# Performance work log

Hardware: AMD Instinct MI355X
Metric: run time of the kernel (lower is better)

Reference implementation:

```python
import jax, jax.numpy as jnp
import numpy as np

B, IN, E, H, MO, OUT, K = 32768, 512, 8, 128, 256, 2, 2


def setup_inputs() -> dict:
    key = jax.random.key(0)
    ks = jax.random.split(key, 9)
    g = lambda k, shape, fan: (jax.random.normal(k, shape, jnp.float32) / np.sqrt(fan)).astype(jnp.float32)
    return {
        "num_prop": jax.random.normal(ks[0], (B, IN), jnp.float32),
        "cat_prop": jax.random.normal(ks[1], (B, 3), jnp.float32),
        "w_gate": g(ks[2], (IN, E), IN),
        "W1": g(ks[3], (E, IN, H), IN),
        "b1": jnp.zeros((E, H), jnp.float32),
        "W2": g(ks[4], (E, H, MO), H),
        "b2": jnp.zeros((E, MO), jnp.float32),
        "Wout": g(ks[5], (MO, OUT), MO),
        "bout": jnp.zeros((OUT,), jnp.float32),
    }


def _cv_squared(v):
    # torch.var is unbiased (ddof=1); eps = 1e-10
    return jnp.var(v, ddof=1) / (jnp.mean(v) ** 2 + 1e-10)


def reference(num_prop, cat_prop, w_gate, W1, b1, W2, b2, Wout, bout):
    b = num_prop.shape[0]
    x = num_prop  # eval mode: dropout is identity, gating noise disabled
    # --- top-k gating ---
    logits = x @ w_gate                                   # [B, E]
    top_vals, top_idx = jax.lax.top_k(logits, K)          # [B, K]
    gate_vals = jax.nn.softmax(top_vals, axis=-1)         # softmax over top-k logits
    gates = jnp.zeros_like(logits).at[jnp.arange(b)[:, None], top_idx].add(gate_vals)  # [B, E]
    # --- load-balancing loss ---
    importance = gates.sum(axis=0)                        # [E]
    load = (gates > 0).astype(jnp.float32).sum(axis=0)    # [E]
    loss = (_cv_squared(importance) + _cv_squared(load)) * 1e-2
    # --- experts (dense-equivalent: gates zero out non-selected experts) ---
    h = jax.nn.relu(jnp.einsum('bi,eih->beh', x, W1) + b1)          # [B, E, H]
    eo = jax.nn.softmax(jnp.einsum('beh,ehm->bem', h, W2) + b2, axis=-1)  # [B, E, MO]
    y = jnp.einsum('be,bem->bm', gates, eo)               # [B, MO]
    # --- output head ---
    out = y @ Wout + bout                                 # [B, OUT]
    return out, loss
```

## Files before the change

### kernel.cpp

```cpp
#include <hip/hip_runtime.h>

#define BN 32768
#define IN 512
#define NE 8
#define NH 128
#define MO 256

typedef const __attribute__((address_space(1))) unsigned int gu32;
typedef __attribute__((address_space(3))) unsigned int lu32;
typedef __attribute__((ext_vector_type(8))) short bf16x8;
typedef __attribute__((ext_vector_type(4))) float f32x4;

__device__ __forceinline__ void cp16(const float* g, float* l) {
    __builtin_amdgcn_global_load_lds((gu32*)g, (lu32*)l, 16, 0, 0);
}

__device__ __forceinline__ unsigned short f2bf(float f) {
    unsigned int u = __float_as_uint(f);
    u = (u + 0x7fffu + ((u >> 16) & 1u)) >> 16;
    return (unsigned short)u;
}
__device__ __forceinline__ float bf2f(unsigned short h) {
    return __uint_as_float((unsigned int)h << 16);
}

__global__ __launch_bounds__(256) void gate_kernel(
    const float* __restrict__ x, const float* __restrict__ wg,
    int* __restrict__ gcount, int* __restrict__ gload, float* __restrict__ gimp,
    int* __restrict__ idx_list, float* __restrict__ gate_list,
    float* __restrict__ out, const float* __restrict__ bout)
{
    __shared__ __align__(16) char wb[32768];
    __shared__ int counts_s[NE];
    __shared__ int load_s[NE];
    __shared__ float imp_s[NE];
    __shared__ int base_s[NE];
    __shared__ int rec_e[128];
    __shared__ int rec_p[128];
    __shared__ float rec_g[128];

    int tid = threadIdx.x;
    if (tid < NE) { counts_s[tid] = 0; load_s[tid] = 0; imp_s[tid] = 0.f; }
    if (tid < 128) {
        int row = blockIdx.x * 64 + (tid >> 1);
        out[row * 2 + (tid & 1)] = bout[tid & 1];
    }
    for (int idx = tid; idx < 1024; idx += 256) {
        int ks = idx >> 6, ls = idx & 63;
        int col = ls & 15;
        int kb = 32 * ks + 8 * (ls >> 4);
        unsigned int ph[4], pl[4];
        #pragma unroll
        for (int j = 0; j < 4; ++j) {
            float v0 = (col < 8) ? wg[(kb + 2 * j) * NE + col] : 0.f;
            float v1 = (col < 8) ? wg[(kb + 2 * j + 1) * NE + col] : 0.f;
            unsigned short h0 = f2bf(v0), h1 = f2bf(v1);
            unsigned short l0 = f2bf(v0 - bf2f(h0)), l1 = f2bf(v1 - bf2f(h1));
            ph[j] = (unsigned int)h0 | ((unsigned int)h1 << 16);
            pl[j] = (unsigned int)l0 | ((unsigned int)l1 << 16);
        }
        *(int4*)(wb + ks * 1024 + ls * 16) = make_int4(ph[0], ph[1], ph[2], ph[3]);
        *(int4*)(wb + 16384 + ks * 1024 + ls * 16) = make_int4(pl[0], pl[1], pl[2], pl[3]);
    }
    __syncthreads();

    int w = tid >> 6, l = tid & 63;
    int e = l & 15;
    int rowA = blockIdx.x * 64 + w * 16 + e;
    const float* px = x + (size_t)rowA * IN + 8 * (l >> 4);

    f32x4 acc = {};
    #pragma unroll
    for (int ks = 0; ks < 16; ++ks) {
        float4 qa = *(const float4*)(px + 32 * ks);
        float4 qb = *(const float4*)(px + 32 * ks + 4);
        float v[8] = {qa.x, qa.y, qa.z, qa.w, qb.x, qb.y, qb.z, qb.w};
        bf16x8 ah, al;
        #pragma unroll
        for (int i = 0; i < 8; ++i) {
            unsigned short h = f2bf(v[i]);
            ah[i] = (short)h;
            al[i] = (short)f2bf(v[i] - bf2f(h));
        }
        bf16x8 bh = *(const bf16x8*)(wb + ks * 1024 + l * 16);
        bf16x8 bl = *(const bf16x8*)(wb + 16384 + ks * 1024 + l * 16);
        acc = __builtin_amdgcn_mfma_f32_16x16x32_bf16(ah, bh, acc, 0, 0, 0);
        acc = __builtin_amdgcn_mfma_f32_16x16x32_bf16(ah, bl, acc, 0, 0, 0);
        acc = __builtin_amdgcn_mfma_f32_16x16x32_bf16(al, bh, acc, 0, 0, 0);
    }

    #pragma unroll
    for (int reg = 0; reg < 4; ++reg) {
        int rloc = w * 16 + 4 * (l >> 4) + reg;
        int row = blockIdx.x * 64 + rloc;
        float lv = (e < 8) ? acc[reg] : -1e30f;

        float v0 = lv; int e0 = e;
        #pragma unroll
        for (int m = 1; m < 8; m <<= 1) {
            float vo = __shfl_xor(v0, m, 64);
            int eo = __shfl_xor(e0, m, 64);
            if (vo > v0 || (vo == v0 && eo < e0)) { v0 = vo; e0 = eo; }
        }
        float v1 = (e == e0 || e >= 8) ? -1e30f : lv; int e1 = e;
        #pragma unroll
        for (int m = 1; m < 8; m <<= 1) {
            float vo = __shfl_xor(v1, m, 64);
            int eo = __shfl_xor(e1, m, 64);
            if (vo > v1 || (vo == v1 && eo < e1)) { v1 = vo; e1 = eo; }
        }
        float v2 = (e == e0 || e == e1 || e >= 8) ? -1e30f : lv;
        #pragma unroll
        for (int m = 1; m < 8; m <<= 1) v2 = fmaxf(v2, __shfl_xor(v2, m, 64));

        double dv0 = v0, dv1 = v1;
        int f0 = e0, f1 = e1;
        if (e < 8 && v1 - v2 < 2e-4f) {
            const float* xr = x + (size_t)row * IN;
            double d0 = 0, d1 = 0, d2 = 0, d3 = 0;
            for (int k = 0; k < IN; k += 4) {
                float4 xv = *(const float4*)(xr + k);
                d0 = fma((double)xv.x, (double)wg[(k    ) * NE + e], d0);
                d1 = fma((double)xv.y, (double)wg[(k + 1) * NE + e], d1);
                d2 = fma((double)xv.z, (double)wg[(k + 2) * NE + e], d2);
                d3 = fma((double)xv.w, (double)wg[(k + 3) * NE + e], d3);
            }
            double ad = (d0 + d1) + (d2 + d3);
            double w0 = ad; int g0i = e;
            #pragma unroll
            for (int m = 1; m < 8; m <<= 1) {
                double vo = __shfl_xor(w0, m, 64);
                int eo = __shfl_xor(g0i, m, 64);
                if (vo > w0 || (vo == w0 && eo < g0i)) { w0 = vo; g0i = eo; }
            }
            double w1 = (e == g0i) ? -1.0e300 : ad; int g1i = e;
            #pragma unroll
            for (int m = 1; m < 8; m <<= 1) {
                double vo = __shfl_xor(w1, m, 64);
                int eo = __shfl_xor(g1i, m, 64);
                if (vo > w1 || (vo == w1 && eo < g1i)) { w1 = vo; g1i = eo; }
            }
            dv0 = w0; dv1 = w1; f0 = g0i; f1 = g1i;
        }

        if (e == 0) {
            float t1 = expf((float)(dv1 - dv0));
            float s = 1.f + t1;
            float g0 = 1.f / s;
            float g1 = t1 / s;
            atomicAdd(&imp_s[f0], g0);
            atomicAdd(&imp_s[f1], g1);
            if (g0 > 0.f) atomicAdd(&load_s[f0], 1);
            if (g1 > 0.f) atomicAdd(&load_s[f1], 1);
            int p0 = atomicAdd(&counts_s[f0], 1);
            int p1 = atomicAdd(&counts_s[f1], 1);
            int rl = rloc * 2;
            rec_e[rl] = f0; rec_e[rl + 1] = f1;
            rec_g[rl] = g0; rec_g[rl + 1] = g1;
            rec_p[rl] = p0; rec_p[rl + 1] = p1;
        }
    }
    __syncthreads();
    if (tid < NE) {
        base_s[tid] = atomicAdd(&gcount[tid], counts_s[tid]);
        atomicAdd(&gimp[tid], imp_s[tid]);
        atomicAdd(&gload[tid], load_s[tid]);
    }
    __syncthreads();
    if (tid < 128) {
        int ee = rec_e[tid];
        int pos = base_s[ee] + rec_p[tid];
        int rw = blockIdx.x * 64 + (tid >> 1);
        idx_list[ee * BN + pos] = rw;
        gate_list[ee * BN + pos] = rec_g[tid];
    }
}

__global__ __launch_bounds__(256) void prep_kernel(
    const float* __restrict__ W1, const float* __restrict__ W2,
    float* __restrict__ W1F, float* __restrict__ W2F)
{
    __shared__ __align__(16) char pb[32768];
    int t = threadIdx.x, b = blockIdx.x;
    if (b < 64) {
        int e = b >> 3, kt = b & 7;
        const float* src = W1 + ((size_t)e * IN + kt * 64) * NH;
        #pragma unroll
        for (int p = 0; p < 8; ++p) {
            int li = p * 256 + t;
            float4 q = *(const float4*)(src + li * 4);
            int kl = li >> 5, n0 = (li & 31) * 4;
            int ks = kl >> 5, g = (kl >> 3) & 3, kb = (kl & 7) * 2;
            float vv[4] = {q.x, q.y, q.z, q.w};
            #pragma unroll
            for (int j = 0; j < 4; ++j) {
                int n = n0 + j;
                int off = (((ks * 8 + (n >> 4)) * 64) + (n & 15) + 16 * g) * 16 + kb;
                unsigned short hh = f2bf(vv[j]);
                unsigned short hl = f2bf(vv[j] - bf2f(hh));
                *(unsigned short*)(pb + off) = hh;
                *(unsigned short*)(pb + 16384 + off) = hl;
            }
        }
        __syncthreads();
        float* dst = W1F + (size_t)b * 8192;
        #pragma unroll
        for (int p = 0; p < 8; ++p) {
            int li = p * 256 + t;
            *(int4*)(dst + li * 4) = *(const int4*)(pb + li * 16);
        }
    } else if (b < 96) {
        int bi = b - 64;
        int e = bi >> 2, kt = bi & 3;
        const float* src = W2 + ((size_t)e * NH + kt * 32) * MO;
        #pragma unroll
        for (int p = 0; p < 8; ++p) {
            int li = p * 256 + t;
            float4 q = *(const float4*)(src + li * 4);
            int kl = li >> 6, n0 = (li & 63) * 4;
            int g = kl >> 3, kb = (kl & 7) * 2;
            float vv[4] = {q.x, q.y, q.z, q.w};
            #pragma unroll
            for (int j = 0; j < 4; ++j) {
                int n = n0 + j;
                int off = ((n >> 4) * 64 + (n & 15) + 16 * g) * 16 + kb;
                unsigned short hh = f2bf(vv[j]);
                unsigned short hl = f2bf(vv[j] - bf2f(hh));
                *(unsigned short*)(pb + off) = hh;
                *(unsigned short*)(pb + 16384 + off) = hl;
            }
        }
        __syncthreads();
        float* dst = W2F + (size_t)bi * 8192;
        #pragma unroll
        for (int p = 0; p < 8; ++p) {
            int li = p * 256 + t;
            *(int4*)(dst + li * 4) = *(const int4*)(pb + li * 16);
        }
    }
}

#define OFF_AH 0
#define OFF_AL 8192
#define OFF_B1 16384
#define OFF_HH 0
#define OFF_HL 16384
#define OFF_B2 32768

__global__ __launch_bounds__(256, 2) void expert_kernel(
    const float* __restrict__ x,
    const float* __restrict__ b1, const float* __restrict__ b2,
    const float* __restrict__ Wout,
    const float* __restrict__ W1F, const float* __restrict__ W2F,
    const int* __restrict__ gcount,
    const float* __restrict__ gimp, const int* __restrict__ gload,
    const int* __restrict__ idx_list, const float* __restrict__ gate_list,
    float* __restrict__ out)
{
    __shared__ __align__(16) char smx[66560];
    __shared__ float woutS[512];

    int e = blockIdx.y;
    int cnt = gcount[e];
    int row0 = blockIdx.x * 64;
    if (e == 0 && blockIdx.x == 0 && threadIdx.x == 0) {
        float mi = 0.f, ml = 0.f;
        for (int k = 0; k < NE; ++k) { mi += gimp[k]; ml += (float)gload[k]; }
        mi *= 0.125f; ml *= 0.125f;
        float vi = 0.f, vl = 0.f;
        for (int k = 0; k < NE; ++k) {
            float d = gimp[k] - mi;  vi += d * d;
            float d2 = (float)gload[k] - ml; vl += d2 * d2;
        }
        vi *= (1.f / 7.f); vl *= (1.f / 7.f);
        out[BN * 2] = (vi / (mi * mi + 1e-10f) + vl / (ml * ml + 1e-10f)) * 0.01f;
    }
    if (row0 >= cnt) return;
    int t = threadIdx.x;
    int l = t & 63, w = t >> 6;

    woutS[t] = Wout[t];
    woutS[256 + t] = Wout[256 + t];

    int s_mf = t >> 6;
    int s_r  = t & 15;
    int s_g  = (t >> 4) & 3;
    int rloc = s_mf * 16 + s_r;
    int sgi = row0 + rloc; if (sgi >= cnt) sgi = cnt - 1;
    const float* xrow = x + (size_t)idx_list[e * BN + sgi] * IN;

    int mbase = (w & 1) * 2;
    int nsel  = w >> 1;

    f32x4 acc1[2][4] = {};
    for (int kt = 0; kt < 8; ++kt) {
        {
            const float* gb = W1F + (size_t)(e * 8 + kt) * 8192;
            float* lb = (float*)(smx + OFF_B1);
            #pragma unroll
            for (int p = 0; p < 8; ++p)
                cp16(gb + (p * 256 + t) * 4, lb + (p * 256 + t) * 4);
        }
        #pragma unroll
        for (int ks = 0; ks < 2; ++ks) {
            int k = kt * 64 + ks * 32 + s_g * 8;
            float4 qa = *(const float4*)(xrow + k);
            float4 qb = *(const float4*)(xrow + k + 4);
            float vv[8] = {qa.x, qa.y, qa.z, qa.w, qb.x, qb.y, qb.z, qb.w};
            unsigned int dh[4], dl[4];
            #pragma unroll
            for (int j = 0; j < 4; ++j) {
                unsigned short h0 = f2bf(vv[2 * j]);
                unsigned short h1 = f2bf(vv[2 * j + 1]);
                unsigned short l0 = f2bf(vv[2 * j] - bf2f(h0));
                unsigned short l1 = f2bf(vv[2 * j + 1] - bf2f(h1));
                dh[j] = (unsigned int)h0 | ((unsigned int)h1 << 16);
                dl[j] = (unsigned int)l0 | ((unsigned int)l1 << 16);
            }
            int slot = ((ks * 4 + s_mf) * 64 + (s_r + 16 * s_g)) * 16;
            *(int4*)(smx + OFF_AH + slot) = make_int4(dh[0], dh[1], dh[2], dh[3]);
            *(int4*)(smx + OFF_AL + slot) = make_int4(dl[0], dl[1], dl[2], dl[3]);
        }
        __syncthreads();
        #pragma unroll
        for (int ks = 0; ks < 2; ++ks) {
            bf16x8 ah[2], al[2];
            #pragma unroll
            for (int mf = 0; mf < 2; ++mf) {
                int ao = ((ks * 4 + mbase + mf) * 64 + l) * 16;
                ah[mf] = *(const bf16x8*)(smx + OFF_AH + ao);
                al[mf] = *(const bf16x8*)(smx + OFF_AL + ao);
            }
            #pragma unroll
            for (int nf = 0; nf < 4; ++nf) {
                int bo = ((ks * 8 + nsel * 4 + nf) * 64 + l) * 16;
                bf16x8 bh = *(const bf16x8*)(smx + OFF_B1 + bo);
                bf16x8 bl = *(const bf16x8*)(smx + OFF_B1 + 16384 + bo);
                #pragma unroll
                for (int mf = 0; mf < 2; ++mf) {
                    acc1[mf][nf] = __builtin_amdgcn_mfma_f32_16x16x32_bf16(ah[mf], bh, acc1[mf][nf], 0, 0, 0);
                    acc1[mf][nf] = __builtin_amdgcn_mfma_f32_16x16x32_bf16(ah[mf], bl, acc1[mf][nf], 0, 0, 0);
                    acc1[mf][nf] = __builtin_amdgcn_mfma_f32_16x16x32_bf16(al[mf], bh, acc1[mf][nf], 0, 0, 0);
                    acc1[mf][nf] = __builtin_amdgcn_mfma_f32_16x16x32_bf16(al[mf], bl, acc1[mf][nf], 0, 0, 0);
                }
            }
        }
        __syncthreads();
    }

    #pragma unroll
    for (int mf = 0; mf < 2; ++mf) {
        int mf2 = (w & 1) * 2 + mf;
        int rlow = 4 * (l >> 4);
        #pragma unroll
        for (int nf = 0; nf < 4; ++nf) {
            int c = nsel * 64 + nf * 16 + (l & 15);
            float b1v = b1[e * NH + c];
            int ks2 = c >> 5;
            int g2 = (c >> 3) & 3;
            int boff = ((ks2 * 4 + mf2) * 64) * 16 + (c & 7) * 2;
            #pragma unroll
            for (int rg = 0; rg < 4; ++rg) {
                float v = fmaxf(acc1[mf][nf][rg] + b1v, 0.f);
                unsigned short hh = f2bf(v);
                unsigned short hl = f2bf(v - bf2f(hh));
                int off = boff + ((rlow + rg) + 16 * g2) * 16;
                *(unsigned short*)(smx + OFF_HH + off) = hh;
                *(unsigned short*)(smx + OFF_HL + off) = hl;
            }
        }
    }
    __syncthreads();

    f32x4 acc2[2][8] = {};
    for (int kt2 = 0; kt2 < 4; ++kt2) {
        {
            const float* gb = W2F + (size_t)(e * 4 + kt2) * 8192;
            float* lb = (float*)(smx + OFF_B2);
            #pragma unroll
            for (int p = 0; p < 8; ++p)
                cp16(gb + (p * 256 + t) * 4, lb + (p * 256 + t) * 4);
        }
        __syncthreads();
        bf16x8 ah[2], al[2];
        #pragma unroll
        for (int mf = 0; mf < 2; ++mf) {
            int ao = ((kt2 * 4 + (w & 1) * 2 + mf) * 64 + l) * 16;
            ah[mf] = *(const bf16x8*)(smx + OFF_HH + ao);
            al[mf] = *(const bf16x8*)(smx + OFF_HL + ao);
        }
        #pragma unroll
        for (int nf = 0; nf < 8; ++nf) {
            int bo = ((nsel * 8 + nf) * 64 + l) * 16;
            bf16x8 bh = *(const bf16x8*)(smx + OFF_B2 + bo);
            bf16x8 bl = *(const bf16x8*)(smx + OFF_B2 + 16384 + bo);
            #pragma unroll
            for (int mf = 0; mf < 2; ++mf) {
                acc2[mf][nf] = __builtin_amdgcn_mfma_f32_16x16x32_bf16(ah[mf], bh, acc2[mf][nf], 0, 0, 0);
                acc2[mf][nf] = __builtin_amdgcn_mfma_f32_16x16x32_bf16(ah[mf], bl, acc2[mf][nf], 0, 0, 0);
                acc2[mf][nf] = __builtin_amdgcn_mfma_f32_16x16x32_bf16(al[mf], bh, acc2[mf][nf], 0, 0, 0);
                acc2[mf][nf] = __builtin_amdgcn_mfma_f32_16x16x32_bf16(al[mf], bl, acc2[mf][nf], 0, 0, 0);
            }
        }
        __syncthreads();
    }

    float* zl = (float*)smx;
    #pragma unroll
    for (int mf = 0; mf < 2; ++mf) {
        int rbase = (w & 1) * 32 + mf * 16 + 4 * (l >> 4);
        #pragma unroll
        for (int nf = 0; nf < 8; ++nf) {
            int c = nsel * 128 + nf * 16 + (l & 15);
            float b2v = b2[e * MO + c];
            #pragma unroll
            for (int rg = 0; rg < 4; ++rg)
                zl[(rbase + rg) * 260 + c] = acc2[mf][nf][rg] + b2v;
        }
    }
    __syncthreads();

    int rr = w * 16 + (l >> 2);
    int c0 = l & 3;
    float vreg[64];
    float m = -1e30f;
    #pragma unroll
    for (int j = 0; j < 64; ++j) {
        vreg[j] = zl[rr * 260 + c0 + 4 * j];
        m = fmaxf(m, vreg[j]);
    }
    m = fmaxf(m, __shfl_xor(m, 1, 64));
    m = fmaxf(m, __shfl_xor(m, 2, 64));
    float s = 0.f, o0 = 0.f, o1 = 0.f;
    #pragma unroll
    for (int j = 0; j < 64; ++j) {
        float tt = __expf(vreg[j] - m);
        s += tt;
        float2 wv = *(const float2*)&woutS[(c0 + 4 * j) * 2];
        o0 = fmaf(tt, wv.x, o0);
        o1 = fmaf(tt, wv.y, o1);
    }
    s  += __shfl_xor(s, 1, 64);  s  += __shfl_xor(s, 2, 64);
    o0 += __shfl_xor(o0, 1, 64); o0 += __shfl_xor(o0, 2, 64);
    o1 += __shfl_xor(o1, 1, 64); o1 += __shfl_xor(o1, 2, 64);
    if (c0 == 0) {
        int gi = row0 + rr;
        if (gi < cnt) {
            float g = gate_list[e * BN + gi];
            int brow = idx_list[e * BN + gi];
            float inv = 1.f / s;
            atomicAdd(&out[brow * 2 + 0], g * o0 * inv);
            atomicAdd(&out[brow * 2 + 1], g * o1 * inv);
        }
    }
}

extern "C" void kernel_launch(void* const* d_in, const int* in_sizes, int n_in,
                              void* d_out, int out_size, void* d_ws, size_t ws_size,
                              hipStream_t stream) {
    const float* x    = (const float*)d_in[0];
    const float* wg   = (const float*)d_in[2];
    const float* W1   = (const float*)d_in[3];
    const float* b1   = (const float*)d_in[4];
    const float* W2   = (const float*)d_in[5];
    const float* b2   = (const float*)d_in[6];
    const float* Wout = (const float*)d_in[7];
    const float* bout = (const float*)d_in[8];
    float* out = (float*)d_out;

    char* ws = (char*)d_ws;
    int*   gcount    = (int*)(ws + 0);
    int*   gload     = (int*)(ws + 32);
    float* gimp      = (float*)(ws + 64);
    int*   idx_list  = (int*)(ws + 128);
    float* gate_list = (float*)(ws + 128 + sizeof(int) * NE * BN);
    float* W1F       = (float*)(ws + 128 + 8 * NE * BN);
    float* W2F       = (float*)(ws + 128 + 8 * NE * BN + 64 * 32768);

    hipMemsetAsync(ws, 0, 128, stream);
    prep_kernel<<<96, 256, 0, stream>>>(W1, W2, W1F, W2F);
    gate_kernel<<<BN / 64, 256, 0, stream>>>(x, wg, gcount, gload, gimp,
                                             idx_list, gate_list, out, bout);
    dim3 eg(BN / 64, NE);
    expert_kernel<<<eg, 256, 0, stream>>>(x, b1, b2, Wout, W1F, W2F,
                                          gcount, gimp, gload,
                                          idx_list, gate_list, out);
}
```

Baseline: 216.6 us.

## Merge weight prep into gate kernel and double-buffer 128-row expert tiles

The weight-splitting prep work now runs as extra blocks of the gate kernel, removing one launch. The expert kernel uses 512 threads over 128-row tiles and double-buffers both the activation and weight tiles in LDS, so the next k-slice loads while MFMAs run. The softmax/output head now works directly from accumulator registers with cross-wave reductions through small LDS arrays, instead of spilling logits to LDS. This doubles LDS use per block to 128 KB, which may limit occupancy, and adds extra barriers.

```diff
diff --git a/kernel.cpp b/kernel.cpp
--- a/kernel.cpp
+++ b/kernel.cpp
@@ -24,8 +24,10 @@
     return __uint_as_float((unsigned int)h << 16);
 }
 
-__global__ __launch_bounds__(256) void gate_kernel(
+__global__ __launch_bounds__(256) void gatep_kernel(
     const float* __restrict__ x, const float* __restrict__ wg,
+    const float* __restrict__ W1, const float* __restrict__ W2,
+    float* __restrict__ W1F, float* __restrict__ W2F,
     int* __restrict__ gcount, int* __restrict__ gload, float* __restrict__ gimp,
     int* __restrict__ idx_list, float* __restrict__ gate_list,
     float* __restrict__ out, const float* __restrict__ bout)
@@ -40,9 +42,73 @@
     __shared__ float rec_g[128];
 
     int tid = threadIdx.x;
+    int bx = blockIdx.x;
+
+    if (bx >= 512) {
+        char* pb = wb;
+        int t = tid, b = bx - 512;
+        if (b < 64) {
+            int e = b >> 3, kt = b & 7;
+            const float* src = W1 + ((size_t)e * IN + kt * 64) * NH;
+            #pragma unroll
+            for (int p = 0; p < 8; ++p) {
+                int li = p * 256 + t;
+                float4 q = *(const float4*)(src + li * 4);
+                int kl = li >> 5, n0 = (li & 31) * 4;
+                int ks = kl >> 5, g = (kl >> 3) & 3, kb = (kl & 7) * 2;
+                float vv[4] = {q.x, q.y, q.z, q.w};
+                #pragma unroll
+                for (int j = 0; j < 4; ++j) {
+                    int n = n0 + j;
+                    int off = (((ks * 8 + (n >> 4)) * 64) + (n & 15) + 16 * g) * 16 + kb;
+                    unsigned short hh = f2bf(vv[j]);
+                    unsigned short hl = f2bf(vv[j] - bf2f(hh));
+                    *(unsigned short*)(pb + off) = hh;
+                    *(unsigned short*)(pb + 16384 + off) = hl;
+                }
+            }
+            __syncthreads();
+            float* dst = W1F + (size_t)b * 8192;
+            #pragma unroll
+            for (int p = 0; p < 8; ++p) {
+                int li = p * 256 + t;
+                *(int4*)(dst + li * 4) = *(const int4*)(pb + li * 16);
+            }
+        } else {
+            int bi = b - 64;
+            int e = bi >> 2, kt = bi & 3;
+            const float* src = W2 + ((size_t)e * NH + kt * 32) * MO;
+            #pragma unroll
+            for (int p = 0; p < 8; ++p) {
+                int li = p * 256 + t;
+                float4 q = *(const float4*)(src + li * 4);
+                int kl = li >> 6, n0 = (li & 63) * 4;
+                int g = kl >> 3, kb = (kl & 7) * 2;
+                float vv[4] = {q.x, q.y, q.z, q.w};
+                #pragma unroll
+                for (int j = 0; j < 4; ++j) {
+                    int n = n0 + j;
+                    int off = ((n >> 4) * 64 + (n & 15) + 16 * g) * 16 + kb;
+                    unsigned short hh = f2bf(vv[j]);
+                    unsigned short hl = f2bf(vv[j] - bf2f(hh));
+                    *(unsigned short*)(pb + off) = hh;
+                    *(unsigned short*)(pb + 16384 + off) = hl;
+                }
+            }
+            __syncthreads();
+            float* dst = W2F + (size_t)bi * 8192;
+            #pragma unroll
+            for (int p = 0; p < 8; ++p) {
+                int li = p * 256 + t;
+                *(int4*)(dst + li * 4) = *(const int4*)(pb + li * 16);
+            }
+        }
+        return;
+    }
+
     if (tid < NE) { counts_s[tid] = 0; load_s[tid] = 0; imp_s[tid] = 0.f; }
     if (tid < 128) {
-        int row = blockIdx.x * 64 + (tid >> 1);
+        int row = bx * 64 + (tid >> 1);
         out[row * 2 + (tid & 1)] = bout[tid & 1];
     }
     for (int idx = tid; idx < 1024; idx += 256) {
@@ -66,7 +132,7 @@
 
     int w = tid >> 6, l = tid & 63;
     int e = l & 15;
-    int rowA = blockIdx.x * 64 + w * 16 + e;
+    int rowA = bx * 64 + w * 16 + e;
     const float* px = x + (size_t)rowA * IN + 8 * (l >> 4);
 
     f32x4 acc = {};
@@ -92,7 +158,7 @@
     #pragma unroll
     for (int reg = 0; reg < 4; ++reg) {
         int rloc = w * 16 + 4 * (l >> 4) + reg;
-        int row = blockIdx.x * 64 + rloc;
+        int row = bx * 64 + rloc;
         float lv = (e < 8) ? acc[reg] : -1e30f;
 
         float v0 = lv; int e0 = e;
@@ -170,84 +236,18 @@
     if (tid < 128) {
         int ee = rec_e[tid];
         int pos = base_s[ee] + rec_p[tid];
-        int rw = blockIdx.x * 64 + (tid >> 1);
+        int rw = bx * 64 + (tid >> 1);
         idx_list[ee * BN + pos] = rw;
         gate_list[ee * BN + pos] = rec_g[tid];
     }
 }
 
-__global__ __launch_bounds__(256) void prep_kernel(
-    const float* __restrict__ W1, const float* __restrict__ W2,
-    float* __restrict__ W1F, float* __restrict__ W2F)
-{
-    __shared__ __align__(16) char pb[32768];
-    int t = threadIdx.x, b = blockIdx.x;
-    if (b < 64) {
-        int e = b >> 3, kt = b & 7;
-        const float* src = W1 + ((size_t)e * IN + kt * 64) * NH;
-        #pragma unroll
-        for (int p = 0; p < 8; ++p) {
-            int li = p * 256 + t;
-            float4 q = *(const float4*)(src + li * 4);
-            int kl = li >> 5, n0 = (li & 31) * 4;
-            int ks = kl >> 5, g = (kl >> 3) & 3, kb = (kl & 7) * 2;
-            float vv[4] = {q.x, q.y, q.z, q.w};
-            #pragma unroll
-            for (int j = 0; j < 4; ++j) {
-                int n = n0 + j;
-                int off = (((ks * 8 + (n >> 4)) * 64) + (n & 15) + 16 * g) * 16 + kb;
-                unsigned short hh = f2bf(vv[j]);
-                unsigned short hl = f2bf(vv[j] - bf2f(hh));
-                *(unsigned short*)(pb + off) = hh;
-                *(unsigned short*)(pb + 16384 + off) = hl;
-            }
-        }
-        __syncthreads();
-        float* dst = W1F + (size_t)b * 8192;
-        #pragma unroll
-        for (int p = 0; p < 8; ++p) {
-            int li = p * 256 + t;
-            *(int4*)(dst + li * 4) = *(const int4*)(pb + li * 16);
-        }
-    } else if (b < 96) {
-        int bi = b - 64;
-        int e = bi >> 2, kt = bi & 3;
-        const float* src = W2 + ((size_t)e * NH + kt * 32) * MO;
-        #pragma unroll
-        for (int p = 0; p < 8; ++p) {
-            int li = p * 256 + t;
-            float4 q = *(const float4*)(src + li * 4);
-            int kl = li >> 6, n0 = (li & 63) * 4;
-            int g = kl >> 3, kb = (kl & 7) * 2;
-            float vv[4] = {q.x, q.y, q.z, q.w};
-            #pragma unroll
-            for (int j = 0; j < 4; ++j) {
-                int n = n0 + j;
-                int off = ((n >> 4) * 64 + (n & 15) + 16 * g) * 16 + kb;
-                unsigned short hh = f2bf(vv[j]);
-                unsigned short hl = f2bf(vv[j] - bf2f(hh));
-                *(unsigned short*)(pb + off) = hh;
-                *(unsigned short*)(pb + 16384 + off) = hl;
-            }
-        }
-        __syncthreads();
-        float* dst = W2F + (size_t)bi * 8192;
-        #pragma unroll
-        for (int p = 0; p < 8; ++p) {
-            int li = p * 256 + t;
-            *(int4*)(dst + li * 4) = *(const int4*)(pb + li * 16);
-        }
-    }
-}
-
-#define OFF_AH 0
-#define OFF_AL 8192
-#define OFF_B1 16384
-#define OFF_HH 0
-#define OFF_HL 16384
-#define OFF_B2 32768
-
-__global__ __launch_bounds__(256, 2) void expert_kernel(
+#define A0 0
+#define A1 32768
+#define WB0 65536
+#define WB1 98304
+
+__global__ __launch_bounds__(512, 2) void expert_kernel(
     const float* __restrict__ x,
     const float* __restrict__ b1, const float* __restrict__ b2,
     const float* __restrict__ Wout,
@@ -257,12 +257,14 @@
     const int* __restrict__ idx_list, const float* __restrict__ gate_list,
     float* __restrict__ out)
 {
-    __shared__ __align__(16) char smx[66560];
+    __shared__ __align__(16) char smx[131072];
     __shared__ float woutS[512];
+    __shared__ float redm[128][2];
+    __shared__ float red3[128][2][3];
 
     int e = blockIdx.y;
     int cnt = gcount[e];
-    int row0 = blockIdx.x * 64;
+    int row0 = blockIdx.x * 128;
     if (e == 0 && blockIdx.x == 0 && threadIdx.x == 0) {
         float mi = 0.f, ml = 0.f;
         for (int k = 0; k < NE; ++k) { mi += gimp[k]; ml += (float)gload[k]; }
@@ -278,32 +280,28 @@
     if (row0 >= cnt) return;
     int t = threadIdx.x;
     int l = t & 63, w = t >> 6;
+    int mq = w & 3;
+    int nh = w >> 2;
 
     woutS[t] = Wout[t];
-    woutS[256 + t] = Wout[256 + t];
 
     int s_mf = t >> 6;
     int s_r  = t & 15;
     int s_g  = (t >> 4) & 3;
-    int rloc = s_mf * 16 + s_r;
-    int sgi = row0 + rloc; if (sgi >= cnt) sgi = cnt - 1;
+    int rloc_s = s_mf * 16 + s_r;
+    int sgi = row0 + rloc_s; if (sgi >= cnt) sgi = cnt - 1;
     const float* xrow = x + (size_t)idx_list[e * BN + sgi] * IN;
 
-    int mbase = (w & 1) * 2;
-    int nsel  = w >> 1;
-
-    f32x4 acc1[2][4] = {};
-    for (int kt = 0; kt < 8; ++kt) {
-        {
-            const float* gb = W1F + (size_t)(e * 8 + kt) * 8192;
-            float* lb = (float*)(smx + OFF_B1);
-            #pragma unroll
-            for (int p = 0; p < 8; ++p)
-                cp16(gb + (p * 256 + t) * 4, lb + (p * 256 + t) * 4);
-        }
+    const float* W1e = W1F + (size_t)e * 65536;
+    const float* W2e = W2F + (size_t)e * 32768;
+
+    {
+        #pragma unroll
+        for (int p = 0; p < 4; ++p)
+            cp16(W1e + (p * 512 + t) * 4, (float*)(smx + WB0) + (p * 512 + t) * 4);
         #pragma unroll
         for (int ks = 0; ks < 2; ++ks) {
-            int k = kt * 64 + ks * 32 + s_g * 8;
+            int k = ks * 32 + s_g * 8;
             float4 qa = *(const float4*)(xrow + k);
             float4 qb = *(const float4*)(xrow + k + 4);
             float vv[8] = {qa.x, qa.y, qa.z, qa.w, qb.x, qb.y, qb.z, qb.w};
@@ -317,25 +315,52 @@
                 dh[j] = (unsigned int)h0 | ((unsigned int)h1 << 16);
                 dl[j] = (unsigned int)l0 | ((unsigned int)l1 << 16);
             }
-            int slot = ((ks * 4 + s_mf) * 64 + (s_r + 16 * s_g)) * 16;
-            *(int4*)(smx + OFF_AH + slot) = make_int4(dh[0], dh[1], dh[2], dh[3]);
-            *(int4*)(smx + OFF_AL + slot) = make_int4(dl[0], dl[1], dl[2], dl[3]);
-        }
-        __syncthreads();
+            int slot = ((ks * 8 + s_mf) * 64 + (s_r + 16 * s_g)) * 16;
+            *(int4*)(smx + A0 + slot) = make_int4(dh[0], dh[1], dh[2], dh[3]);
+            *(int4*)(smx + A0 + 16384 + slot) = make_int4(dl[0], dl[1], dl[2], dl[3]);
+        }
+    }
+    __syncthreads();
+
+    f32x4 acc1[2][4] = {};
+    for (int kt = 0; kt < 8; ++kt) {
+        char* acur = smx + ((kt & 1) ? A1 : A0);
+        char* wcur = smx + ((kt & 1) ? WB1 : WB0);
+        char* anx  = smx + ((kt & 1) ? A0 : A1);
+        char* wnx  = smx + ((kt & 1) ? WB0 : WB1);
+
+        float4 ra[2][2];
+        if (kt < 7) {
+            #pragma unroll
+            for (int ks = 0; ks < 2; ++ks) {
+                int k = (kt + 1) * 64 + ks * 32 + s_g * 8;
+                ra[ks][0] = *(const float4*)(xrow + k);
+                ra[ks][1] = *(const float4*)(xrow + k + 4);
+            }
+            const float* gb = W1e + (size_t)(kt + 1) * 8192;
+            #pragma unroll
+            for (int p = 0; p < 4; ++p)
+                cp16(gb + (p * 512 + t) * 4, (float*)wnx + (p * 512 + t) * 4);
+        } else {
+            #pragma unroll
+            for (int p = 0; p < 4; ++p)
+                cp16(W2e + (p * 512 + t) * 4, (float*)wnx + (p * 512 + t) * 4);
+        }
+
         #pragma unroll
         for (int ks = 0; ks < 2; ++ks) {
             bf16x8 ah[2], al[2];
             #pragma unroll
             for (int mf = 0; mf < 2; ++mf) {
-                int ao = ((ks * 4 + mbase + mf) * 64 + l) * 16;
-                ah[mf] = *(const bf16x8*)(smx + OFF_AH + ao);
-                al[mf] = *(const bf16x8*)(smx + OFF_AL + ao);
+                int ao = ((ks * 8 + mq * 2 + mf) * 64 + l) * 16;
+                ah[mf] = *(const bf16x8*)(acur + ao);
+                al[mf] = *(const bf16x8*)(acur + 16384 + ao);
             }
             #pragma unroll
             for (int nf = 0; nf < 4; ++nf) {
-                int bo = ((ks * 8 + nsel * 4 + nf) * 64 + l) * 16;
-                bf16x8 bh = *(const bf16x8*)(smx + OFF_B1 + bo);
-                bf16x8 bl = *(const bf16x8*)(smx + OFF_B1 + 16384 + bo);
+                int bo = ((ks * 8 + nh * 4 + nf) * 64 + l) * 16;
+                bf16x8 bh = *(const bf16x8*)(wcur + bo);
+                bf16x8 bl = *(const bf16x8*)(wcur + 16384 + bo);
                 #pragma unroll
                 for (int mf = 0; mf < 2; ++mf) {
                     acc1[mf][nf] = __builtin_amdgcn_mfma_f32_16x16x32_bf16(ah[mf], bh, acc1[mf][nf], 0, 0, 0);
@@ -345,28 +370,49 @@
                 }
             }
         }
+
+        if (kt < 7) {
+            #pragma unroll
+            for (int ks = 0; ks < 2; ++ks) {
+                float vv[8] = {ra[ks][0].x, ra[ks][0].y, ra[ks][0].z, ra[ks][0].w,
+                               ra[ks][1].x, ra[ks][1].y, ra[ks][1].z, ra[ks][1].w};
+                unsigned int dh[4], dl[4];
+                #pragma unroll
+                for (int j = 0; j < 4; ++j) {
+                    unsigned short h0 = f2bf(vv[2 * j]);
+                    unsigned short h1 = f2bf(vv[2 * j + 1]);
+                    unsigned short l0 = f2bf(vv[2 * j] - bf2f(h0));
+                    unsigned short l1 = f2bf(vv[2 * j + 1] - bf2f(h1));
+                    dh[j] = (unsigned int)h0 | ((unsigned int)h1 << 16);
+                    dl[j] = (unsigned int)l0 | ((unsigned int)l1 << 16);
+                }
+                int slot = ((ks * 8 + s_mf) * 64 + (s_r + 16 * s_g)) * 16;
+                *(int4*)(anx + slot) = make_int4(dh[0], dh[1], dh[2], dh[3]);
+                *(int4*)(anx + 16384 + slot) = make_int4(dl[0], dl[1], dl[2], dl[3]);
+            }
+        }
         __syncthreads();
     }
 
     #pragma unroll
     for (int mf = 0; mf < 2; ++mf) {
-        int mf2 = (w & 1) * 2 + mf;
+        int mf2 = mq * 2 + mf;
         int rlow = 4 * (l >> 4);
         #pragma unroll
         for (int nf = 0; nf < 4; ++nf) {
-            int c = nsel * 64 + nf * 16 + (l & 15);
+            int c = nh * 64 + nf * 16 + (l & 15);
             float b1v = b1[e * NH + c];
-            int ks2 = c >> 5;
+            int kt2c = c >> 5;
             int g2 = (c >> 3) & 3;
-            int boff = ((ks2 * 4 + mf2) * 64) * 16 + (c & 7) * 2;
+            int boff = ((kt2c * 8 + mf2) * 64) * 16 + (c & 7) * 2;
             #pragma unroll
             for (int rg = 0; rg < 4; ++rg) {
                 float v = fmaxf(acc1[mf][nf][rg] + b1v, 0.f);
                 unsigned short hh = f2bf(v);
                 unsigned short hl = f2bf(v - bf2f(hh));
                 int off = boff + ((rlow + rg) + 16 * g2) * 16;
-                *(unsigned short*)(smx + OFF_HH + off) = hh;
-                *(unsigned short*)(smx + OFF_HL + off) = hl;
+                *(unsigned short*)(smx + off) = hh;
+                *(unsigned short*)(smx + 32768 + off) = hl;
             }
         }
     }
@@ -374,84 +420,109 @@
 
     f32x4 acc2[2][8] = {};
     for (int kt2 = 0; kt2 < 4; ++kt2) {
-        {
-            const float* gb = W2F + (size_t)(e * 4 + kt2) * 8192;
-            float* lb = (float*)(smx + OFF_B2);
-            #pragma unroll
-            for (int p = 0; p < 8; ++p)
-                cp16(gb + (p * 256 + t) * 4, lb + (p * 256 + t) * 4);
+        char* wcur = smx + ((kt2 & 1) ? WB1 : WB0);
+        char* wnx  = smx + ((kt2 & 1) ? WB0 : WB1);
+        if (kt2 < 3) {
+            const float* gb = W2e + (size_t)(kt2 + 1) * 8192;
+            #pragma unroll
+            for (int p = 0; p < 4; ++p)
+                cp16(gb + (p * 512 + t) * 4, (float*)wnx + (p * 512 + t) * 4);
+        }
+        bf16x8 ah2[2], al2[2];
+        #pragma unroll
+        for (int mf = 0; mf < 2; ++mf) {
+            int ao = ((kt2 * 8 + mq * 2 + mf) * 64 + l) * 16;
+            ah2[mf] = *(const bf16x8*)(smx + ao);
+            al2[mf] = *(const bf16x8*)(smx + 32768 + ao);
+        }
+        #pragma unroll
+        for (int nf = 0; nf < 8; ++nf) {
+            int bo = ((nh * 8 + nf) * 64 + l) * 16;
+            bf16x8 bh = *(const bf16x8*)(wcur + bo);
+            bf16x8 bl = *(const bf16x8*)(wcur + 16384 + bo);
+            #pragma unroll
+            for (int mf = 0; mf < 2; ++mf) {
+                acc2[mf][nf] = __builtin_amdgcn_mfma_f32_16x16x32_bf16(ah2[mf], bh, acc2[mf][nf], 0, 0, 0);
+                acc2[mf][nf] = __builtin_amdgcn_mfma_f32_16x16x32_bf16(ah2[mf], bl, acc2[mf][nf], 0, 0, 0);
+                acc2[mf][nf] = __builtin_amdgcn_mfma_f32_16x16x32_bf16(al2[mf], bh, acc2[mf][nf], 0, 0, 0);
+                acc2[mf][nf] = __builtin_amdgcn_mfma_f32_16x16x32_bf16(al2[mf], bl, acc2[mf][nf], 0, 0, 0);
+            }
         }
         __syncthreads();
-        bf16x8 ah[2], al[2];
-        #pragma unroll
-        for (int mf = 0; mf < 2; ++mf) {
-            int ao = ((kt2 * 4 + (w & 1) * 2 + mf) * 64 + l) * 16;
-            ah[mf] = *(const bf16x8*)(smx + OFF_HH + ao);
-            al[mf] = *(const bf16x8*)(smx + OFF_HL + ao);
-        }
-        #pragma unroll
-        for (int nf = 0; nf < 8; ++nf) {
-            int bo = ((nsel * 8 + nf) * 64 + l) * 16;
-            bf16x8 bh = *(const bf16x8*)(smx + OFF_B2 + bo);
-            bf16x8 bl = *(const bf16x8*)(smx + OFF_B2 + 16384 + bo);
-            #pragma unroll
-            for (int mf = 0; mf < 2; ++mf) {
-                acc2[mf][nf] = __builtin_amdgcn_mfma_f32_16x16x32_bf16(ah[mf], bh, acc2[mf][nf], 0, 0, 0);
-                acc2[mf][nf] = __builtin_amdgcn_mfma_f32_16x16x32_bf16(ah[mf], bl, acc2[mf][nf], 0, 0, 0);
-                acc2[mf][nf] = __builtin_amdgcn_mfma_f32_16x16x32_bf16(al[mf], bh, acc2[mf][nf], 0, 0, 0);
-                acc2[mf][nf] = __builtin_amdgcn_mfma_f32_16x16x32_bf16(al[mf], bl, acc2[mf][nf], 0, 0, 0);
-            }
-        }
-        __syncthreads();
-    }
-
-    float* zl = (float*)smx;
+    }
+
+    float2 wrow[8];
     #pragma unroll
-    for (int mf = 0; mf < 2; ++mf) {
-        int rbase = (w & 1) * 32 + mf * 16 + 4 * (l >> 4);
-        #pragma unroll
-        for (int nf = 0; nf < 8; ++nf) {
-            int c = nsel * 128 + nf * 16 + (l & 15);
-            float b2v = b2[e * MO + c];
-            #pragma unroll
-            for (int rg = 0; rg < 4; ++rg)
-                zl[(rbase + rg) * 260 + c] = acc2[mf][nf][rg] + b2v;
-        }
-    }
-    __syncthreads();
-
-    int rr = w * 16 + (l >> 2);
-    int c0 = l & 3;
-    float vreg[64];
-    float m = -1e30f;
+    for (int nf = 0; nf < 8; ++nf) {
+        int c = nh * 128 + nf * 16 + (l & 15);
+        float b2v = b2[e * MO + c];
+        #pragma unroll
+        for (int rg = 0; rg < 4; ++rg) {
+            acc2[0][nf][rg] += b2v;
+            acc2[1][nf][rg] += b2v;
+        }
+        wrow[nf] = *(const float2*)&woutS[2 * c];
+    }
     #pragma unroll
-    for (int j = 0; j < 64; ++j) {
-        vreg[j] = zl[rr * 260 + c0 + 4 * j];
-        m = fmaxf(m, vreg[j]);
-    }
-    m = fmaxf(m, __shfl_xor(m, 1, 64));
-    m = fmaxf(m, __shfl_xor(m, 2, 64));
-    float s = 0.f, o0 = 0.f, o1 = 0.f;
+    for (int mf = 0; mf < 2; ++mf)
+        #pragma unroll
+        for (int rg = 0; rg < 4; ++rg) {
+            float m = -1e30f;
+            #pragma unroll
+            for (int nf = 0; nf < 8; ++nf) m = fmaxf(m, acc2[mf][nf][rg]);
+            m = fmaxf(m, __shfl_xor(m, 1, 64));
+            m = fmaxf(m, __shfl_xor(m, 2, 64));
+            m = fmaxf(m, __shfl_xor(m, 4, 64));
+            m = fmaxf(m, __shfl_xor(m, 8, 64));
+            int rloc = mq * 32 + mf * 16 + 4 * (l >> 4) + rg;
+            if ((l & 15) == 0) redm[rloc][nh] = m;
+        }
+    __syncthreads();
     #pragma unroll
-    for (int j = 0; j < 64; ++j) {
-        float tt = __expf(vreg[j] - m);
-        s += tt;
-        float2 wv = *(const float2*)&woutS[(c0 + 4 * j) * 2];
-        o0 = fmaf(tt, wv.x, o0);
-        o1 = fmaf(tt, wv.y, o1);
-    }
-    s  += __shfl_xor(s, 1, 64);  s  += __shfl_xor(s, 2, 64);
-    o0 += __shfl_xor(o0, 1, 64); o0 += __shfl_xor(o0, 2, 64);
-    o1 += __shfl_xor(o1, 1, 64); o1 += __shfl_xor(o1, 2, 64);
-    if (c0 == 0) {
-        int gi = row0 + rr;
-        if (gi < cnt) {
-            float g = gate_list[e * BN + gi];
-            int brow = idx_list[e * BN + gi];
-            float inv = 1.f / s;
-            atomicAdd(&out[brow * 2 + 0], g * o0 * inv);
-            atomicAdd(&out[brow * 2 + 1], g * o1 * inv);
-        }
+    for (int mf = 0; mf < 2; ++mf)
+        #pragma unroll
+        for (int rg = 0; rg < 4; ++rg) {
+            int rloc = mq * 32 + mf * 16 + 4 * (l >> 4) + rg;
+            float M = fmaxf(redm[rloc][0], redm[rloc][1]);
+            float s = 0.f, o0 = 0.f, o1 = 0.f;
+            #pragma unroll
+            for (int nf = 0; nf < 8; ++nf) {
+                float tt = __expf(acc2[mf][nf][rg] - M);
+                s += tt;
+                o0 = fmaf(tt, wrow[nf].x, o0);
+                o1 = fmaf(tt, wrow[nf].y, o1);
+            }
+            s += __shfl_xor(s, 1, 64); s += __shfl_xor(s, 2, 64);
+            s += __shfl_xor(s, 4, 64); s += __shfl_xor(s, 8, 64);
+            o0 += __shfl_xor(o0, 1, 64); o0 += __shfl_xor(o0, 2, 64);
+            o0 += __shfl_xor(o0, 4, 64); o0 += __shfl_xor(o0, 8, 64);
+            o1 += __shfl_xor(o1, 1, 64); o1 += __shfl_xor(o1, 2, 64);
+            o1 += __shfl_xor(o1, 4, 64); o1 += __shfl_xor(o1, 8, 64);
+            if ((l & 15) == 0) {
+                red3[rloc][nh][0] = s;
+                red3[rloc][nh][1] = o0;
+                red3[rloc][nh][2] = o1;
+            }
+        }
+    __syncthreads();
+    if (nh == 0 && (l & 15) == 0) {
+        #pragma unroll
+        for (int mf = 0; mf < 2; ++mf)
+            #pragma unroll
+            for (int rg = 0; rg < 4; ++rg) {
+                int rloc = mq * 32 + mf * 16 + 4 * (l >> 4) + rg;
+                float S  = red3[rloc][0][0] + red3[rloc][1][0];
+                float O0 = red3[rloc][0][1] + red3[rloc][1][1];
+                float O1 = red3[rloc][0][2] + red3[rloc][1][2];
+                int gi = row0 + rloc;
+                if (gi < cnt) {
+                    float g = gate_list[e * BN + gi];
+                    int brow = idx_list[e * BN + gi];
+                    float inv = 1.f / S;
+                    atomicAdd(&out[brow * 2 + 0], g * O0 * inv);
+                    atomicAdd(&out[brow * 2 + 1], g * O1 * inv);
+                }
+            }
     }
 }
 
@@ -478,11 +549,11 @@
     float* W2F       = (float*)(ws + 128 + 8 * NE * BN + 64 * 32768);
 
     hipMemsetAsync(ws, 0, 128, stream);
-    prep_kernel<<<96, 256, 0, stream>>>(W1, W2, W1F, W2F);
-    gate_kernel<<<BN / 64, 256, 0, stream>>>(x, wg, gcount, gload, gimp,
-                                             idx_list, gate_list, out, bout);
-    dim3 eg(BN / 64, NE);
-    expert_kernel<<<eg, 256, 0, stream>>>(x, b1, b2, Wout, W1F, W2F,
+    gatep_kernel<<<608, 256, 0, stream>>>(x, wg, W1, W2, W1F, W2F,
+                                          gcount, gload, gimp,
+                                          idx_list, gate_list, out, bout);
+    dim3 eg(BN / 128, NE);
+    expert_kernel<<<eg, 512, 0, stream>>>(x, b1, b2, Wout, W1F, W2F,
                                           gcount, gimp, gload,
                                           idx_list, gate_list, out);
 }
```

New measurement: 245.1 us. +13.2%, slower.
